# Optimization experiments

Hardware: AMD Instinct MI355X
Metric: run time of the kernel (lower is better)

The kernel has to match this reference:

```python
import jax, jax.numpy as jnp
import numpy as np

S = 256
H = 4       # n_heads
DH = 32     # head_dim
D = H * DH  # model dim
EPS = 1e-5


def setup_inputs() -> dict:
    key = jax.random.key(0)
    ks = jax.random.split(key, 12)
    x = jax.random.normal(ks[0], (1, S, S, D), dtype=jnp.float32)
    # attention mask: mostly 0, occasionally large negative (masked)
    keep = jax.random.uniform(ks[1], (1, 1, S, S)) < 0.9
    attn_mask = jnp.where(keep, 0.0, -1e9).astype(jnp.float32)
    sc = 1.0 / np.sqrt(D)
    ln_w = jnp.ones((D,), jnp.float32)
    ln_b = jnp.zeros((D,), jnp.float32)
    Wb = jax.random.normal(ks[2], (H, D), jnp.float32) * sc   # bias projection (linear.weight)
    Wq = jax.random.normal(ks[3], (D, D), jnp.float32) * sc
    Wk = jax.random.normal(ks[4], (D, D), jnp.float32) * sc
    Wv = jax.random.normal(ks[5], (D, D), jnp.float32) * sc
    Wg = jax.random.normal(ks[6], (D, D), jnp.float32) * sc
    Wo = jax.random.normal(ks[7], (D, D), jnp.float32) * sc
    return {"x": x, "attn_mask": attn_mask, "ln_w": ln_w, "ln_b": ln_b,
            "Wb": Wb, "Wq": Wq, "Wk": Wk, "Wv": Wv, "Wg": Wg, "Wo": Wo}


def reference(x, attn_mask, ln_w, ln_b, Wb, Wq, Wk, Wv, Wg, Wo):
    # x: [1,S,S,D] pair representation; ending=False so no transpose of S axes.
    x0 = x[0]  # [S,S,D]
    mu = jnp.mean(x0, axis=-1, keepdims=True)
    var = jnp.mean(jnp.square(x0 - mu), axis=-1, keepdims=True)
    xn = (x0 - mu) * jax.lax.rsqrt(var + EPS) * ln_w + ln_b  # [S,S,D]

    # triangle bias: [S,S,H] -> [1,H,S,S] (broadcast over batch-of-rows)
    bias = jnp.einsum('bqd,hd->hbq', xn, Wb)[None]  # [1,H,S,S]

    def heads(W):
        return jnp.einsum('bqd,ed->bqe', xn, W).reshape(S, S, H, DH).transpose(0, 2, 1, 3)

    q, k, v = heads(Wq), heads(Wk), heads(Wv)  # each [S,H,S,DH]

    scale = 1.0 / np.sqrt(DH)
    scores = jnp.einsum('bhqd,bhkd->bhqk', q, k) * scale + bias + attn_mask  # [S,H,S,S]
    attn = jax.nn.softmax(scores, axis=-1)
    o = jnp.einsum('bhqk,bhkd->bhqd', attn, v)  # [S,H,S,DH]
    o = o.transpose(0, 2, 1, 3).reshape(S, S, D)

    g = jnp.einsum('bqd,ed->bqe', xn, Wg)
    out = jnp.einsum('bqe,fe->bqf', o * jax.nn.sigmoid(g), Wo)  # [S,S,D]
    return out[None]  # [1,S,S,D]
```

## Files before the change

### kernel.cpp

```cpp
#include <hip/hip_runtime.h>
#include <hip/hip_bf16.h>

#define S_DIM 256
#define D_DIM 128
#define H_DIM 4
#define NPOS  (S_DIM * S_DIM)

typedef __attribute__((ext_vector_type(8))) short  short8;
typedef __attribute__((ext_vector_type(4))) float  f32x4;

__device__ __forceinline__ float b2f(unsigned short u) {
    union { float f; unsigned int u32; } c; c.u32 = ((unsigned int)u) << 16; return c.f;
}
__device__ __forceinline__ unsigned short f2b(float f) {
    __hip_bfloat16 h = __float2bfloat16(f);
    return *reinterpret_cast<unsigned short*>(&h);
}

__global__ __launch_bounds__(256) void ln_biasxn_kernel(
    const float* __restrict__ x, const float* __restrict__ mask,
    const float* __restrict__ lnw, const float* __restrict__ lnb,
    const float* __restrict__ Wb,
    float* __restrict__ bm, unsigned short* __restrict__ xn)
{
    const int wave = threadIdx.x >> 6, lane = threadIdx.x & 63;
    const int p = blockIdx.x * 4 + wave;

    float2 v = ((const float2*)x)[p * 64 + lane];
    float s = v.x + v.y, ss = v.x * v.x + v.y * v.y;
    #pragma unroll
    for (int m = 1; m < 64; m <<= 1) { s += __shfl_xor(s, m); ss += __shfl_xor(ss, m); }
    float mean = s * (1.f / 128.f);
    float var  = ss * (1.f / 128.f) - mean * mean;
    float rstd = rsqrtf(var + 1e-5f);

    float xn0 = (v.x - mean) * rstd * lnw[lane * 2]     + lnb[lane * 2];
    float xn1 = (v.y - mean) * rstd * lnw[lane * 2 + 1] + lnb[lane * 2 + 1];
    ((unsigned int*)xn)[p * 64 + lane] =
        (unsigned int)f2b(xn0) | ((unsigned int)f2b(xn1) << 16);

    float mval = mask[p];
    #pragma unroll
    for (int h = 0; h < H_DIM; h++) {
        float d = xn0 * Wb[h * 128 + lane * 2] + xn1 * Wb[h * 128 + lane * 2 + 1];
        #pragma unroll
        for (int m = 1; m < 64; m <<= 1) d += __shfl_xor(d, m);
        if (lane == 0) bm[(long)h * NPOS + p] = d + mval;
    }
}

__global__ __launch_bounds__(256) void proj_mfma_kernel(
    const unsigned short* __restrict__ xn,
    const float* __restrict__ Wq, const float* __restrict__ Wk,
    const float* __restrict__ Wv, const float* __restrict__ Wg,
    int h, unsigned short* __restrict__ qkvg)
{
    __shared__ __align__(16) unsigned short A_lds[64 * 136];
    __shared__ __align__(16) unsigned short W_lds[128 * 136];
    const int tid = threadIdx.x;
    const int m0 = blockIdx.x * 64;

    const int lr = tid >> 4, c8 = (tid & 15) * 8;
    #pragma unroll
    for (int i = 0; i < 4; i++) {
        uint4 t = *(const uint4*)(xn + (size_t)(m0 + lr + i * 16) * 128 + c8);
        *(uint4*)(&A_lds[(lr + i * 16) * 136 + c8]) = t;
    }
    #pragma unroll
    for (int i = 0; i < 8; i++) {
        int wr = lr + i * 16;
        const float* Ws = (wr < 32) ? Wq : (wr < 64) ? Wk : (wr < 96) ? Wv : Wg;
        const float* src = Ws + (size_t)(h * 32 + (wr & 31)) * 128 + c8;
        float4 f0 = *(const float4*)(src);
        float4 f1 = *(const float4*)(src + 4);
        unsigned short pk[8] = {f2b(f0.x), f2b(f0.y), f2b(f0.z), f2b(f0.w),
                                f2b(f1.x), f2b(f1.y), f2b(f1.z), f2b(f1.w)};
        *(uint4*)(&W_lds[wr * 136 + c8]) = *(const uint4*)pk;
    }
    __syncthreads();

    const int w = tid >> 6, lane = tid & 63;
    const int l16 = lane & 15, quad = lane >> 4;
    f32x4 acc[8];
    #pragma unroll
    for (int nt = 0; nt < 8; nt++) acc[nt] = (f32x4){0.f, 0.f, 0.f, 0.f};

    #pragma unroll
    for (int k0 = 0; k0 < 128; k0 += 32) {
        short8 a = *(const short8*)(&A_lds[(w * 16 + l16) * 136 + k0 + quad * 8]);
        #pragma unroll
        for (int nt = 0; nt < 8; nt++) {
            short8 b = *(const short8*)(&W_lds[(nt * 16 + l16) * 136 + k0 + quad * 8]);
            acc[nt] = __builtin_amdgcn_mfma_f32_16x16x32_bf16(a, b, acc[nt], 0, 0, 0);
        }
    }

    #pragma unroll
    for (int nt = 0; nt < 8; nt++)
        #pragma unroll
        for (int rr = 0; rr < 4; rr++) {
            int row = m0 + w * 16 + quad * 4 + rr;
            qkvg[(size_t)row * 128 + nt * 16 + l16] = f2b(acc[nt][rr]);
        }
}

__global__ __launch_bounds__(256) void attn_mfma_kernel(
    const unsigned short* __restrict__ qkvg, const float* __restrict__ bm,
    int h, float* __restrict__ out)
{
    __shared__ __align__(16) unsigned short VT_lds[32 * 264];
    __shared__ __align__(16) unsigned short P_lds[4 * 16 * 264];
    const int b = blockIdx.x;
    const int tid = threadIdx.x;

    {
        const int row = tid >> 2, chunk = (tid & 3) * 8;
        #pragma unroll
        for (int i = 0; i < 4; i++) {
            int rr = row + i * 64;
            uint4 v = *(const uint4*)(qkvg + (size_t)(b * 256 + rr) * 128 + 64 + chunk);
            unsigned short vs[8] = {
                (unsigned short)(v.x & 0xffff), (unsigned short)(v.x >> 16),
                (unsigned short)(v.y & 0xffff), (unsigned short)(v.y >> 16),
                (unsigned short)(v.z & 0xffff), (unsigned short)(v.z >> 16),
                (unsigned short)(v.w & 0xffff), (unsigned short)(v.w >> 16)};
            #pragma unroll
            for (int j = 0; j < 8; j++) VT_lds[(chunk + j) * 264 + rr] = vs[j];
        }
    }
    __syncthreads();

    const int w = tid >> 6, lane = tid & 63;
    const int l16 = lane & 15, quad = lane >> 4;
    const float* bmh = bm + (long)h * NPOS;
    unsigned short* P_w = P_lds + w * 16 * 264;
    const float scale = 0.17677669529663687f;

    #pragma unroll 1
    for (int i = 0; i < 4; i++) {
        const int q0 = (w * 4 + i) * 16;
        short8 aq = *(const short8*)(qkvg + (size_t)(b * 256 + q0 + l16) * 128 + quad * 8);

        float sc[16][4];
        #pragma unroll
        for (int nt = 0; nt < 16; nt++) {
            short8 kb = *(const short8*)(qkvg + (size_t)(b * 256 + nt * 16 + l16) * 128 + 32 + quad * 8);
            f32x4 c = (f32x4){0.f, 0.f, 0.f, 0.f};
            c = __builtin_amdgcn_mfma_f32_16x16x32_bf16(aq, kb, c, 0, 0, 0);
            #pragma unroll
            for (int rr = 0; rr < 4; rr++) {
                int row = q0 + quad * 4 + rr;
                sc[nt][rr] = c[rr] * scale + bmh[(long)row * 256 + nt * 16 + l16];
            }
        }
        float rsum[4];
        #pragma unroll
        for (int rr = 0; rr < 4; rr++) {
            float m = sc[0][rr];
            #pragma unroll
            for (int nt = 1; nt < 16; nt++) m = fmaxf(m, sc[nt][rr]);
            #pragma unroll
            for (int msk = 1; msk < 16; msk <<= 1) m = fmaxf(m, __shfl_xor(m, msk));
            float ssum = 0.f;
            #pragma unroll
            for (int nt = 0; nt < 16; nt++) {
                float pv = __expf(sc[nt][rr] - m);
                sc[nt][rr] = pv; ssum += pv;
            }
            #pragma unroll
            for (int msk = 1; msk < 16; msk <<= 1) ssum += __shfl_xor(ssum, msk);
            rsum[rr] = ssum;
        }
        #pragma unroll
        for (int nt = 0; nt < 16; nt++)
            #pragma unroll
            for (int rr = 0; rr < 4; rr++)
                P_w[(quad * 4 + rr) * 264 + nt * 16 + l16] = f2b(sc[nt][rr]);

        f32x4 oacc[2];
        oacc[0] = (f32x4){0.f, 0.f, 0.f, 0.f};
        oacc[1] = (f32x4){0.f, 0.f, 0.f, 0.f};
        #pragma unroll
        for (int kt = 0; kt < 8; kt++) {
            short8 pa = *(const short8*)(&P_w[l16 * 264 + kt * 32 + quad * 8]);
            #pragma unroll
            for (int nh = 0; nh < 2; nh++) {
                short8 vb = *(const short8*)(&VT_lds[(nh * 16 + l16) * 264 + kt * 32 + quad * 8]);
                oacc[nh] = __builtin_amdgcn_mfma_f32_16x16x32_bf16(pa, vb, oacc[nh], 0, 0, 0);
            }
        }
        #pragma unroll
        for (int rr = 0; rr < 4; rr++) {
            int row = q0 + quad * 4 + rr;
            float inv = 1.f / rsum[rr];
            #pragma unroll
            for (int nh = 0; nh < 2; nh++) {
                int cl = nh * 16 + l16;
                float g = b2f(qkvg[(size_t)(b * 256 + row) * 128 + 96 + cl]);
                float ov = oacc[nh][rr] * inv;
                ov = ov / (1.f + __expf(-g));
                out[((long)b * 256 + row) * 128 + h * 32 + cl] = ov;
            }
        }
    }
}

__global__ __launch_bounds__(256) void outproj_mfma_kernel(
    const float* __restrict__ Wo, float* out)
{
    __shared__ __align__(16) unsigned short A_lds[64 * 136];
    __shared__ __align__(16) unsigned short W_lds[128 * 136];
    const int tid = threadIdx.x;
    const int m0 = blockIdx.x * 64;

    const int lr = tid >> 4, c8 = (tid & 15) * 8;
    #pragma unroll
    for (int i = 0; i < 4; i++) {
        const float* src = out + (size_t)(m0 + lr + i * 16) * 128 + c8;
        float4 f0 = *(const float4*)(src);
        float4 f1 = *(const float4*)(src + 4);
        unsigned short pk[8] = {f2b(f0.x), f2b(f0.y), f2b(f0.z), f2b(f0.w),
                                f2b(f1.x), f2b(f1.y), f2b(f1.z), f2b(f1.w)};
        *(uint4*)(&A_lds[(lr + i * 16) * 136 + c8]) = *(const uint4*)pk;
    }
    #pragma unroll
    for (int i = 0; i < 8; i++) {
        const float* src = Wo + (size_t)(lr + i * 16) * 128 + c8;
        float4 f0 = *(const float4*)(src);
        float4 f1 = *(const float4*)(src + 4);
        unsigned short pk[8] = {f2b(f0.x), f2b(f0.y), f2b(f0.z), f2b(f0.w),
                                f2b(f1.x), f2b(f1.y), f2b(f1.z), f2b(f1.w)};
        *(uint4*)(&W_lds[(lr + i * 16) * 136 + c8]) = *(const uint4*)pk;
    }
    __syncthreads();

    const int w = tid >> 6, lane = tid & 63;
    const int l16 = lane & 15, quad = lane >> 4;
    f32x4 acc[8];
    #pragma unroll
    for (int nt = 0; nt < 8; nt++) acc[nt] = (f32x4){0.f, 0.f, 0.f, 0.f};

    #pragma unroll
    for (int k0 = 0; k0 < 128; k0 += 32) {
        short8 a = *(const short8*)(&A_lds[(w * 16 + l16) * 136 + k0 + quad * 8]);
        #pragma unroll
        for (int nt = 0; nt < 8; nt++) {
            short8 b = *(const short8*)(&W_lds[(nt * 16 + l16) * 136 + k0 + quad * 8]);
            acc[nt] = __builtin_amdgcn_mfma_f32_16x16x32_bf16(a, b, acc[nt], 0, 0, 0);
        }
    }

    #pragma unroll
    for (int nt = 0; nt < 8; nt++)
        #pragma unroll
        for (int rr = 0; rr < 4; rr++) {
            int row = m0 + w * 16 + quad * 4 + rr;
            out[(size_t)row * 128 + nt * 16 + l16] = acc[nt][rr];
        }
}

extern "C" void kernel_launch(void* const* d_in, const int* in_sizes, int n_in,
                              void* d_out, int out_size, void* d_ws, size_t ws_size,
                              hipStream_t stream)
{
    (void)in_sizes; (void)n_in; (void)out_size; (void)ws_size;
    const float* x    = (const float*)d_in[0];
    const float* mask = (const float*)d_in[1];
    const float* lnw  = (const float*)d_in[2];
    const float* lnb  = (const float*)d_in[3];
    const float* Wb   = (const float*)d_in[4];
    const float* Wq   = (const float*)d_in[5];
    const float* Wk   = (const float*)d_in[6];
    const float* Wv   = (const float*)d_in[7];
    const float* Wg   = (const float*)d_in[8];
    const float* Wo   = (const float*)d_in[9];
    float* out = (float*)d_out;

    char* ws = (char*)d_ws;
    float*          bm   = (float*)ws;
    unsigned short* xn   = (unsigned short*)(ws + 1048576);
    unsigned short* qkvg = (unsigned short*)(ws + 1048576 + 16777216);

    ln_biasxn_kernel<<<NPOS / 4, 256, 0, stream>>>(x, mask, lnw, lnb, Wb, bm, xn);
    for (int h = 0; h < H_DIM; h++) {
        proj_mfma_kernel<<<NPOS / 64, 256, 0, stream>>>(xn, Wq, Wk, Wv, Wg, h, qkvg);
        attn_mfma_kernel<<<S_DIM, 256, 0, stream>>>(qkvg, bm, h, out);
    }
    outproj_mfma_kernel<<<NPOS / 64, 256, 0, stream>>>(Wo, out);
}
```

Before: 241.3 us.

## Fuse layernorm into projection and batch all heads per row strip

Removes the bf16 xn intermediate and recomputes layernorm inside the projection kernel, which now computes all four Q/K/V/G matrices across grid.y. It loops over row strips sized to the workspace rather than over heads, so attention runs on all heads in a single launch with four times as many blocks. This cuts kernel launches and the xn round trip and raises attention parallelism, but needs a larger workspace. Layernorm is also recomputed for each of the four projections.

```diff
diff --git a/kernel.cpp b/kernel.cpp
--- a/kernel.cpp
+++ b/kernel.cpp
@@ -17,11 +17,10 @@
     return *reinterpret_cast<unsigned short*>(&h);
 }
 
-__global__ __launch_bounds__(256) void ln_biasxn_kernel(
+__global__ __launch_bounds__(256) void ln_biasmask_kernel(
     const float* __restrict__ x, const float* __restrict__ mask,
     const float* __restrict__ lnw, const float* __restrict__ lnb,
-    const float* __restrict__ Wb,
-    float* __restrict__ bm, unsigned short* __restrict__ xn)
+    const float* __restrict__ Wb, float* __restrict__ bm)
 {
     const int wave = threadIdx.x >> 6, lane = threadIdx.x & 63;
     const int p = blockIdx.x * 4 + wave;
@@ -36,8 +35,6 @@
 
     float xn0 = (v.x - mean) * rstd * lnw[lane * 2]     + lnb[lane * 2];
     float xn1 = (v.y - mean) * rstd * lnw[lane * 2 + 1] + lnb[lane * 2 + 1];
-    ((unsigned int*)xn)[p * 64 + lane] =
-        (unsigned int)f2b(xn0) | ((unsigned int)f2b(xn1) << 16);
 
     float mval = mask[p];
     #pragma unroll
@@ -49,28 +46,46 @@
     }
 }
 
-__global__ __launch_bounds__(256) void proj_mfma_kernel(
-    const unsigned short* __restrict__ xn,
+__global__ __launch_bounds__(256) void proj_ln_kernel(
+    const float* __restrict__ x,
+    const float* __restrict__ lnw, const float* __restrict__ lnb,
     const float* __restrict__ Wq, const float* __restrict__ Wk,
     const float* __restrict__ Wv, const float* __restrict__ Wg,
-    int h, unsigned short* __restrict__ qkvg)
+    int p0, unsigned short* __restrict__ strip)
 {
     __shared__ __align__(16) unsigned short A_lds[64 * 136];
     __shared__ __align__(16) unsigned short W_lds[128 * 136];
     const int tid = threadIdx.x;
     const int m0 = blockIdx.x * 64;
+    const int gy = blockIdx.y;
+    const float* W = (gy == 0) ? Wq : (gy == 1) ? Wk : (gy == 2) ? Wv : Wg;
 
     const int lr = tid >> 4, c8 = (tid & 15) * 8;
     #pragma unroll
     for (int i = 0; i < 4; i++) {
-        uint4 t = *(const uint4*)(xn + (size_t)(m0 + lr + i * 16) * 128 + c8);
-        *(uint4*)(&A_lds[(lr + i * 16) * 136 + c8]) = t;
+        int row = lr + i * 16;
+        const float* src = x + (size_t)(p0 + m0 + row) * 128 + c8;
+        float4 f0 = *(const float4*)(src);
+        float4 f1 = *(const float4*)(src + 4);
+        float s  = f0.x + f0.y + f0.z + f0.w + f1.x + f1.y + f1.z + f1.w;
+        float ss = f0.x*f0.x + f0.y*f0.y + f0.z*f0.z + f0.w*f0.w
+                 + f1.x*f1.x + f1.y*f1.y + f1.z*f1.z + f1.w*f1.w;
+        #pragma unroll
+        for (int m = 1; m < 16; m <<= 1) { s += __shfl_xor(s, m); ss += __shfl_xor(ss, m); }
+        float mean = s * (1.f / 128.f);
+        float var  = ss * (1.f / 128.f) - mean * mean;
+        float rstd = rsqrtf(var + 1e-5f);
+        float xv[8] = {f0.x, f0.y, f0.z, f0.w, f1.x, f1.y, f1.z, f1.w};
+        unsigned short pk[8];
+        #pragma unroll
+        for (int j = 0; j < 8; j++)
+            pk[j] = f2b((xv[j] - mean) * rstd * lnw[c8 + j] + lnb[c8 + j]);
+        *(uint4*)(&A_lds[row * 136 + c8]) = *(const uint4*)pk;
     }
     #pragma unroll
     for (int i = 0; i < 8; i++) {
         int wr = lr + i * 16;
-        const float* Ws = (wr < 32) ? Wq : (wr < 64) ? Wk : (wr < 96) ? Wv : Wg;
-        const float* src = Ws + (size_t)(h * 32 + (wr & 31)) * 128 + c8;
+        const float* src = W + (size_t)wr * 128 + c8;
         float4 f0 = *(const float4*)(src);
         float4 f1 = *(const float4*)(src + 4);
         unsigned short pk[8] = {f2b(f0.x), f2b(f0.y), f2b(f0.z), f2b(f0.w),
@@ -100,17 +115,18 @@
         #pragma unroll
         for (int rr = 0; rr < 4; rr++) {
             int row = m0 + w * 16 + quad * 4 + rr;
-            qkvg[(size_t)row * 128 + nt * 16 + l16] = f2b(acc[nt][rr]);
-        }
-}
-
-__global__ __launch_bounds__(256) void attn_mfma_kernel(
-    const unsigned short* __restrict__ qkvg, const float* __restrict__ bm,
-    int h, float* __restrict__ out)
+            strip[(size_t)row * 512 + gy * 128 + nt * 16 + l16] = f2b(acc[nt][rr]);
+        }
+}
+
+__global__ __launch_bounds__(256) void attn_kernel(
+    const unsigned short* __restrict__ strip, const float* __restrict__ bm,
+    int b0, float* __restrict__ out)
 {
     __shared__ __align__(16) unsigned short VT_lds[32 * 264];
     __shared__ __align__(16) unsigned short P_lds[4 * 16 * 264];
-    const int b = blockIdx.x;
+    const int bl = blockIdx.x, h = blockIdx.y;
+    const int b  = b0 + bl;
     const int tid = threadIdx.x;
 
     {
@@ -118,7 +134,7 @@
         #pragma unroll
         for (int i = 0; i < 4; i++) {
             int rr = row + i * 64;
-            uint4 v = *(const uint4*)(qkvg + (size_t)(b * 256 + rr) * 128 + 64 + chunk);
+            uint4 v = *(const uint4*)(strip + (size_t)(bl * 256 + rr) * 512 + 256 + h * 32 + chunk);
             unsigned short vs[8] = {
                 (unsigned short)(v.x & 0xffff), (unsigned short)(v.x >> 16),
                 (unsigned short)(v.y & 0xffff), (unsigned short)(v.y >> 16),
@@ -139,12 +155,12 @@
     #pragma unroll 1
     for (int i = 0; i < 4; i++) {
         const int q0 = (w * 4 + i) * 16;
-        short8 aq = *(const short8*)(qkvg + (size_t)(b * 256 + q0 + l16) * 128 + quad * 8);
+        short8 aq = *(const short8*)(strip + (size_t)(bl * 256 + q0 + l16) * 512 + h * 32 + quad * 8);
 
         float sc[16][4];
         #pragma unroll
         for (int nt = 0; nt < 16; nt++) {
-            short8 kb = *(const short8*)(qkvg + (size_t)(b * 256 + nt * 16 + l16) * 128 + 32 + quad * 8);
+            short8 kb = *(const short8*)(strip + (size_t)(bl * 256 + nt * 16 + l16) * 512 + 128 + h * 32 + quad * 8);
             f32x4 c = (f32x4){0.f, 0.f, 0.f, 0.f};
             c = __builtin_amdgcn_mfma_f32_16x16x32_bf16(aq, kb, c, 0, 0, 0);
             #pragma unroll
@@ -196,7 +212,7 @@
             #pragma unroll
             for (int nh = 0; nh < 2; nh++) {
                 int cl = nh * 16 + l16;
-                float g = b2f(qkvg[(size_t)(b * 256 + row) * 128 + 96 + cl]);
+                float g = b2f(strip[(size_t)(bl * 256 + row) * 512 + 384 + h * 32 + cl]);
                 float ov = oacc[nh][rr] * inv;
                 ov = ov / (1.f + __expf(-g));
                 out[((long)b * 256 + row) * 128 + h * 32 + cl] = ov;
@@ -263,7 +279,7 @@
                               void* d_out, int out_size, void* d_ws, size_t ws_size,
                               hipStream_t stream)
 {
-    (void)in_sizes; (void)n_in; (void)out_size; (void)ws_size;
+    (void)in_sizes; (void)n_in; (void)out_size;
     const float* x    = (const float*)d_in[0];
     const float* mask = (const float*)d_in[1];
     const float* lnw  = (const float*)d_in[2];
@@ -276,15 +292,19 @@
     const float* Wo   = (const float*)d_in[9];
     float* out = (float*)d_out;
 
+    const size_t bmB = (size_t)H_DIM * NPOS * sizeof(float);
+    int HB = 256;
+    while (HB > 16 && bmB + (size_t)HB * 256 * 512 * 2 > ws_size) HB >>= 1;
+
     char* ws = (char*)d_ws;
-    float*          bm   = (float*)ws;
-    unsigned short* xn   = (unsigned short*)(ws + 1048576);
-    unsigned short* qkvg = (unsigned short*)(ws + 1048576 + 16777216);
-
-    ln_biasxn_kernel<<<NPOS / 4, 256, 0, stream>>>(x, mask, lnw, lnb, Wb, bm, xn);
-    for (int h = 0; h < H_DIM; h++) {
-        proj_mfma_kernel<<<NPOS / 64, 256, 0, stream>>>(xn, Wq, Wk, Wv, Wg, h, qkvg);
-        attn_mfma_kernel<<<S_DIM, 256, 0, stream>>>(qkvg, bm, h, out);
+    float*          bm    = (float*)ws;
+    unsigned short* strip = (unsigned short*)(ws + bmB);
+
+    ln_biasmask_kernel<<<NPOS / 4, 256, 0, stream>>>(x, mask, lnw, lnb, Wb, bm);
+    for (int b0 = 0; b0 < S_DIM; b0 += HB) {
+        proj_ln_kernel<<<dim3(HB * 4, 4), 256, 0, stream>>>(
+            x, lnw, lnb, Wq, Wk, Wv, Wg, b0 * 256, strip);
+        attn_kernel<<<dim3(HB, H_DIM), 256, 0, stream>>>(strip, bm, b0, out);
     }
     outproj_mfma_kernel<<<NPOS / 64, 256, 0, stream>>>(Wo, out);
 }
```

After: 230.4 us. -4.5%, faster.
